# Kernel tuning notes

Hardware: AMD Instinct MI355X
Metric: run time of the kernel (lower is better)

## Reference

```python
import math
import jax, jax.numpy as jnp
import numpy as np

D_MODEL = 512
NHEAD = 8
D_HEAD = D_MODEL // NHEAD
ATTN_TEMP = 1.0
B, LQ, LK = 2, 2048, 4096


def _linear_params(key, d_in, d_out):
    kw, kb = jax.random.split(key)
    bound = 1.0 / math.sqrt(d_in)
    W = jax.random.uniform(kw, (d_out, d_in), jnp.float32, -bound, bound)
    b = jax.random.uniform(kb, (d_out,), jnp.float32, -bound, bound)
    return W, b


def setup_inputs() -> dict:
    key = jax.random.key(0)
    ks = jax.random.split(key, 8)
    q = jax.random.normal(ks[0], (B, LQ, D_MODEL), jnp.float32)
    kv = jax.random.normal(ks[1], (B, LK, D_MODEL), jnp.float32)
    key_gate = jax.random.uniform(ks[2], (B, LK), jnp.float32)
    key_mask = jax.random.randint(ks[3], (B, LK), 0, 2, jnp.int32)
    Wq, bq = _linear_params(ks[4], D_MODEL, D_MODEL)
    Wk, bk = _linear_params(ks[5], D_MODEL, D_MODEL)
    Wv, bv = _linear_params(ks[6], D_MODEL, D_MODEL)
    Wo, bo = _linear_params(ks[7], D_MODEL, D_MODEL)
    return {"q": q, "kv": kv, "key_gate": key_gate, "key_mask": key_mask,
            "Wq": Wq, "bq": bq, "Wk": Wk, "bk": bk,
            "Wv": Wv, "bv": bv, "Wo": Wo, "bo": bo}


def reference(q, kv, key_gate, key_mask, Wq, bq, Wk, bk, Wv, bv, Wo, bo):
    Bq, Lq, _ = q.shape
    _, Lk, _ = kv.shape
    # projections -> (B, H, L, Dh)
    qp = (q @ Wq.T + bq).reshape(Bq, Lq, NHEAD, D_HEAD).transpose(0, 2, 1, 3)
    kp = (kv @ Wk.T + bk).reshape(Bq, Lk, NHEAD, D_HEAD).transpose(0, 2, 1, 3)
    vp = (kv @ Wv.T + bv).reshape(Bq, Lk, NHEAD, D_HEAD).transpose(0, 2, 1, 3)
    # scores: (B, H, Lq, Lk)
    scores = jnp.einsum('bhqd,bhkd->bhqk', qp, kp) / (math.sqrt(D_HEAD) * ATTN_TEMP)
    log_gate = jnp.log(jnp.clip(key_gate, 1e-6, None))  # (B, Lk)
    scores = scores + log_gate[:, None, None, :]
    pad = (key_mask == 0)[:, None, None, :]
    scores = jnp.where(pad, -jnp.inf, scores)
    attn = jax.nn.softmax(scores, axis=-1)  # dropout is identity in eval
    out = jnp.einsum('bhqk,bhkd->bhqd', attn, vp)
    out = out.transpose(0, 2, 1, 3).reshape(Bq, Lq, D_MODEL)
    return out @ Wo.T + bo
```

## Files before the change

kernel.cpp:

```cpp
#include <hip/hip_runtime.h>
#include <hip/hip_bf16.h>


using bf16  = __hip_bfloat16;
using bf16x8 = __attribute__((ext_vector_type(8))) short;
using f32x4  = __attribute__((ext_vector_type(4))) float;

#define MFMA16(a, b, c) __builtin_amdgcn_mfma_f32_16x16x32_bf16((a), (b), (c), 0, 0, 0)

__device__ __forceinline__ bf16x8 load8(const bf16* p) {
    return *reinterpret_cast<const bf16x8*>(p);
}
__device__ __forceinline__ short f2bf(float x) {
    bf16 h = __float2bfloat16(x);
    return *reinterpret_cast<short*>(&h);
}

__global__ void cvt_x(const float* __restrict__ q, const float* __restrict__ kv,
                      bf16* __restrict__ qb, bf16* __restrict__ kvb) {
    int i = blockIdx.x * blockDim.x + threadIdx.x;
    const float* src; bf16* dst; int j;
    if (i < 524288) { src = q;  dst = qb;  j = i; }
    else            { src = kv; dst = kvb; j = i - 524288; }
    float4 v = reinterpret_cast<const float4*>(src)[j];
    ushort4 o;
    o.x = (unsigned short)f2bf(v.x);
    o.y = (unsigned short)f2bf(v.y);
    o.z = (unsigned short)f2bf(v.z);
    o.w = (unsigned short)f2bf(v.w);
    reinterpret_cast<ushort4*>(dst)[j] = o;
}

__global__ void cvt_w(const float* __restrict__ a, const float* __restrict__ b,
                      const float* __restrict__ c, const float* __restrict__ d,
                      bf16* __restrict__ oa, bf16* __restrict__ ob,
                      bf16* __restrict__ oc, bf16* __restrict__ od) {
    int i = blockIdx.x * blockDim.x + threadIdx.x;
    int t = i >> 16, j = i & 65535;
    const float* src = (t == 0) ? a : (t == 1) ? b : (t == 2) ? c : d;
    bf16*        dst = (t == 0) ? oa : (t == 1) ? ob : (t == 2) ? oc : od;
    float4 v = reinterpret_cast<const float4*>(src)[j];
    ushort4 o;
    o.x = (unsigned short)f2bf(v.x);
    o.y = (unsigned short)f2bf(v.y);
    o.z = (unsigned short)f2bf(v.z);
    o.w = (unsigned short)f2bf(v.w);
    reinterpret_cast<ushort4*>(dst)[j] = o;
}

__global__ void prep_gate_kernel(const float* __restrict__ gate,
                                 const int* __restrict__ mask,
                                 float* __restrict__ g, int n) {
    int i = blockIdx.x * blockDim.x + threadIdx.x;
    if (i < n) {
        float gv = fmaxf(gate[i], 1e-6f);
        g[i] = mask[i] ? logf(gv) : -1e30f;
    }
}

__device__ __forceinline__ void proj_body(const bf16* __restrict__ X,
                                          const bf16* __restrict__ W,
                                          const float* __restrict__ bias,
                                          void* __restrict__ Cout,
                                          int mode, int L, int mb, bf16* Ws) {
    const int tid  = threadIdx.x;
    const int wave = tid >> 6;
    const int lane = tid & 63;
    const int li   = lane & 15;
    const int quad = lane >> 4;
    const int n0   = blockIdx.x * 64;
    const int m0   = mb * 128 + wave * 32;

    f32x4 zero = {0.f, 0.f, 0.f, 0.f};
    f32x4 acc[2][4];
    for (int mt = 0; mt < 2; ++mt)
        for (int t = 0; t < 4; ++t) acc[mt][t] = zero;

    const bf16* x0 = X + (size_t)(m0 + li) * 512;
    const bf16* x1 = X + (size_t)(m0 + 16 + li) * 512;

    for (int p = 0; p < 2; ++p) {
        __syncthreads();
        for (int i = 0; i < 8; ++i) {
            const int c  = i * 256 + tid;
            const int cr = c >> 5;
            const int kc = (c & 31) * 8;
            *reinterpret_cast<bf16x8*>(&Ws[cr * 264 + kc]) =
                load8(W + (size_t)(n0 + cr) * 512 + p * 256 + kc);
        }
        __syncthreads();

        for (int k0 = 0; k0 < 256; k0 += 32) {
            bf16x8 a0 = load8(x0 + p * 256 + k0 + quad * 8);
            bf16x8 a1 = load8(x1 + p * 256 + k0 + quad * 8);
            for (int t = 0; t < 4; ++t) {
                bf16x8 w8 = load8(&Ws[(t * 16 + li) * 264 + k0 + quad * 8]);
                acc[0][t] = MFMA16(a0, w8, acc[0][t]);
                acc[1][t] = MFMA16(a1, w8, acc[1][t]);
            }
        }
    }

    for (int t = 0; t < 4; ++t) {
        const int col = n0 + t * 16 + li;
        const float bcol = bias[col];
        for (int mt = 0; mt < 2; ++mt) {
            for (int r = 0; r < 4; ++r) {
                const int row = m0 + mt * 16 + quad * 4 + r;
                const float v = acc[mt][t][r] + bcol;
                if (mode == 0) {
                    ((float*)Cout)[(size_t)row * 512 + col] = v;
                } else {
                    const int bb2 = row / L;
                    const int i   = row - bb2 * L;
                    const int hh  = col >> 6;
                    const int dh  = col & 63;
                    size_t idx;
                    if (mode == 1) idx = ((size_t)(bb2 * 8 + hh) * L + i) * 64 + dh;
                    else           idx = ((size_t)(bb2 * 8 + hh) * 64 + dh) * L + i;
                    ((bf16*)Cout)[idx] = __float2bfloat16(v);
                }
            }
        }
    }
}

__global__ void proj_qkv(const bf16* __restrict__ qb, const bf16* __restrict__ kvb,
                         const bf16* __restrict__ Wq, const float* __restrict__ bq,
                         const bf16* __restrict__ Wk, const float* __restrict__ bk,
                         const bf16* __restrict__ Wv, const float* __restrict__ bv,
                         bf16* __restrict__ qp, bf16* __restrict__ kp,
                         bf16* __restrict__ vpt) {
    __shared__ alignas(16) bf16 Ws[64 * 264];
    const int my = blockIdx.y;
    if (my < 32)      proj_body(qb,  Wq, bq, qp,  1, 2048, my,      Ws);
    else if (my < 96) proj_body(kvb, Wk, bk, kp,  1, 4096, my - 32, Ws);
    else              proj_body(kvb, Wv, bv, vpt, 2, 4096, my - 96, Ws);
}

__global__ void proj_o(const bf16* __restrict__ op, const bf16* __restrict__ Wo,
                       const float* __restrict__ bo, float* __restrict__ out) {
    __shared__ alignas(16) bf16 Ws[64 * 264];
    proj_body(op, Wo, bo, out, 0, 1, blockIdx.y, Ws);
}

#define PS 72
__global__ void attn_kernel(const bf16* __restrict__ qp, const bf16* __restrict__ kp,
                            const bf16* __restrict__ vpt, const float* __restrict__ g,
                            float* __restrict__ Opart, float* __restrict__ lpart) {
    __shared__ alignas(16) bf16 Kt[64 * PS];
    __shared__ alignas(16) bf16 Vt[64 * PS];
    __shared__ alignas(16) bf16 Pt[4 * 32 * PS];
    __shared__ float gs[64];

    const int tid  = threadIdx.x;
    const int wave = tid >> 6;
    const int lane = tid & 63;
    const int li   = lane & 15;
    const int quad = lane >> 4;

    const int bx = blockIdx.x;
    const int ks = bx & 3;
    const int qt = (bx >> 2) & 15;
    const int h  = (bx >> 6) & 7;
    const int b  = bx >> 9;
    const size_t bh = (size_t)(b * 8 + h);

    const bf16* qb0 = qp + (bh * 2048 + (size_t)qt * 128 + wave * 32 + li) * 64;
    bf16x8 aq[2][2];
    aq[0][0] = load8(qb0 + quad * 8);
    aq[0][1] = load8(qb0 + 32 + quad * 8);
    aq[1][0] = load8(qb0 + 16 * 64 + quad * 8);
    aq[1][1] = load8(qb0 + 16 * 64 + 32 + quad * 8);

    f32x4 zero = {0.f, 0.f, 0.f, 0.f};
    f32x4 o[2][4];
    for (int mt = 0; mt < 2; ++mt)
        for (int t = 0; t < 4; ++t) o[mt][t] = zero;
    float lsum[2][4] = {{0.f, 0.f, 0.f, 0.f}, {0.f, 0.f, 0.f, 0.f}};

    const bf16* ksrc  = kp  + bh * 4096 * 64;
    const bf16* vsrc  = vpt + bh * 64 * 4096;
    const float* gsrc = g + (size_t)b * 4096;

    bf16* PtW = &Pt[wave * 32 * PS];

    for (int kt = ks * 16; kt < ks * 16 + 16; ++kt) {
        {
            const int r0 = tid >> 3;
            const int cg = (tid & 7) * 8;
            const bf16* kst = ksrc + (size_t)kt * 64 * 64;
            *reinterpret_cast<bf16x8*>(&Kt[r0 * PS + cg])        = load8(kst + r0 * 64 + cg);
            *reinterpret_cast<bf16x8*>(&Kt[(r0 + 32) * PS + cg]) = load8(kst + (r0 + 32) * 64 + cg);
            const bf16* vs = vsrc + kt * 64;
            *reinterpret_cast<bf16x8*>(&Vt[r0 * PS + cg])        = load8(vs + (size_t)r0 * 4096 + cg);
            *reinterpret_cast<bf16x8*>(&Vt[(r0 + 32) * PS + cg]) = load8(vs + (size_t)(r0 + 32) * 4096 + cg);
            if (tid < 64) gs[tid] = gsrc[kt * 64 + tid];
        }
        __syncthreads();

        for (int t = 0; t < 4; ++t) {
            bf16x8 bk0 = load8(&Kt[(t * 16 + li) * PS + quad * 8]);
            bf16x8 bk1 = load8(&Kt[(t * 16 + li) * PS + 32 + quad * 8]);
            const float gv = gs[t * 16 + li];
            for (int mt = 0; mt < 2; ++mt) {
                f32x4 acc = zero;
                acc = MFMA16(aq[mt][0], bk0, acc);
                acc = MFMA16(aq[mt][1], bk1, acc);
                for (int r = 0; r < 4; ++r) {
                    const float p = __expf(acc[r] * 0.125f + gv);
                    lsum[mt][r] += p;
                    PtW[(mt * 16 + quad * 4 + r) * PS + t * 16 + li] = __float2bfloat16(p);
                }
            }
        }

        bf16x8 ap[2][2];
        ap[0][0] = load8(&PtW[li * PS + quad * 8]);
        ap[0][1] = load8(&PtW[li * PS + 32 + quad * 8]);
        ap[1][0] = load8(&PtW[(16 + li) * PS + quad * 8]);
        ap[1][1] = load8(&PtW[(16 + li) * PS + 32 + quad * 8]);
        for (int t = 0; t < 4; ++t) {
            bf16x8 bv0 = load8(&Vt[(t * 16 + li) * PS + quad * 8]);
            bf16x8 bv1 = load8(&Vt[(t * 16 + li) * PS + 32 + quad * 8]);
            for (int mt = 0; mt < 2; ++mt) {
                o[mt][t] = MFMA16(ap[mt][0], bv0, o[mt][t]);
                o[mt][t] = MFMA16(ap[mt][1], bv1, o[mt][t]);
            }
        }
        __syncthreads();
    }

    for (int off = 1; off < 16; off <<= 1)
        for (int mt = 0; mt < 2; ++mt)
            for (int r = 0; r < 4; ++r)
                lsum[mt][r] += __shfl_xor(lsum[mt][r], off);

    float* ob = Opart + ((size_t)bx * 128 + wave * 32) * 64;
    for (int mt = 0; mt < 2; ++mt)
        for (int t = 0; t < 4; ++t)
            for (int r = 0; r < 4; ++r)
                ob[(size_t)(mt * 16 + quad * 4 + r) * 64 + t * 16 + li] = o[mt][t][r];
    if (li == 0)
        for (int mt = 0; mt < 2; ++mt)
            for (int r = 0; r < 4; ++r)
                lpart[(size_t)bx * 128 + wave * 32 + mt * 16 + quad * 4 + r] = lsum[mt][r];
}

__global__ void attn_combine(const float* __restrict__ Opart,
                             const float* __restrict__ lpart,
                             bf16* __restrict__ op) {
    const int gidx = blockIdx.x * 256 + threadIdx.x;
    const int row  = gidx >> 2;
    const int c0   = (gidx & 3) * 16;
    const int b    = row >> 14;
    const int h    = (row >> 11) & 7;
    const int q    = row & 2047;
    const int qt   = q >> 7;
    const int r128 = q & 127;
    const int base = (((b * 8 + h) * 16) + qt) * 4;

    float acc[16];
    for (int j = 0; j < 16; ++j) acc[j] = 0.f;
    float L = 0.f;
    for (int s = 0; s < 4; ++s) {
        const float* src = Opart + ((size_t)(base + s) * 128 + r128) * 64 + c0;
        const float4 v0 = reinterpret_cast<const float4*>(src)[0];
        const float4 v1 = reinterpret_cast<const float4*>(src)[1];
        const float4 v2 = reinterpret_cast<const float4*>(src)[2];
        const float4 v3 = reinterpret_cast<const float4*>(src)[3];
        acc[0] += v0.x; acc[1] += v0.y; acc[2]  += v0.z; acc[3]  += v0.w;
        acc[4] += v1.x; acc[5] += v1.y; acc[6]  += v1.z; acc[7]  += v1.w;
        acc[8] += v2.x; acc[9] += v2.y; acc[10] += v2.z; acc[11] += v2.w;
        acc[12] += v3.x; acc[13] += v3.y; acc[14] += v3.z; acc[15] += v3.w;
        L += lpart[(size_t)(base + s) * 128 + r128];
    }
    const float invL = 1.0f / L;

    bf16* dst = op + ((size_t)b * 2048 + q) * 512 + h * 64 + c0;
    bf16x8 r0, r1;
    for (int j = 0; j < 8; ++j) {
        r0[j] = f2bf(acc[j] * invL);
        r1[j] = f2bf(acc[8 + j] * invL);
    }
    *reinterpret_cast<bf16x8*>(dst)     = r0;
    *reinterpret_cast<bf16x8*>(dst + 8) = r1;
}

extern "C" void kernel_launch(void* const* d_in, const int* in_sizes, int n_in,
                              void* d_out, int out_size, void* d_ws, size_t ws_size,
                              hipStream_t stream) {
    const float* q    = (const float*)d_in[0];
    const float* kv   = (const float*)d_in[1];
    const float* gate = (const float*)d_in[2];
    const int*   mask = (const int*)d_in[3];
    const float* Wq = (const float*)d_in[4];  const float* bq = (const float*)d_in[5];
    const float* Wk = (const float*)d_in[6];  const float* bk = (const float*)d_in[7];
    const float* Wv = (const float*)d_in[8];  const float* bv = (const float*)d_in[9];
    const float* Wo = (const float*)d_in[10]; const float* bo = (const float*)d_in[11];
    float* out = (float*)d_out;

    char* ws = (char*)d_ws;
    float* g   = (float*)ws;
    bf16* Wqb  = (bf16*)(ws + (1u  << 20));
    bf16* Wkb  = (bf16*)(ws + (1u  << 20) + (512u << 10));
    bf16* Wvb  = (bf16*)(ws + (2u  << 20));
    bf16* Wob  = (bf16*)(ws + (2u  << 20) + (512u << 10));
    bf16* qb   = (bf16*)(ws + (3u  << 20));
    bf16* kvb  = (bf16*)(ws + (7u  << 20));
    bf16* qp   = (bf16*)(ws + (15u << 20));
    bf16* kp   = (bf16*)(ws + (19u << 20));
    bf16* vpt  = (bf16*)(ws + (27u << 20));
    bf16* op   = (bf16*)(ws + (35u << 20));
    float* Opart = (float*)(ws + (39u << 20));
    float* lpart = (float*)(ws + (71u << 20));

    prep_gate_kernel<<<32, 256, 0, stream>>>(gate, mask, g, 2 * 4096);
    cvt_x<<<6144, 256, 0, stream>>>(q, kv, qb, kvb);
    cvt_w<<<1024, 256, 0, stream>>>(Wq, Wk, Wv, Wo, Wqb, Wkb, Wvb, Wob);

    proj_qkv<<<dim3(8, 160), 256, 0, stream>>>(qb, kvb, Wqb, bq, Wkb, bk,
                                               Wvb, bv, qp, kp, vpt);

    attn_kernel<<<1024, 256, 0, stream>>>(qp, kp, vpt, g, Opart, lpart);
    attn_combine<<<512, 256, 0, stream>>>(Opart, lpart, op);

    proj_o<<<dim3(8, 32), 256, 0, stream>>>(op, Wob, bo, out);
}
```

Before: 202.1 us.

## Rewrite attention with 32x32 MFMA, fragment-ordered K/V layouts and register-resident P

The projection kernel now writes K and V directly in MFMA fragment order, so the attention kernel loads operands straight from global memory into registers with no LDS staging and no block barriers. Attention switches to 32x32x16 MFMAs, computes S^T so P can be repacked in registers with cvt_pk_bf16 and permlane32_swap, and uses exp2 with a log2 gate. It prefetches the next K tile while running the PV MFMAs, and the partial-output layout changes so the combine kernel reads contiguous rows. The cost is higher register pressure, tied to launch_bounds of 2 blocks, and fewer blocks (512) each covering 256 queries.

```diff
diff --git a/kernel.cpp b/kernel.cpp
--- a/kernel.cpp
+++ b/kernel.cpp
@@ -2,11 +2,14 @@
 #include <hip/hip_bf16.h>
 
 
-using bf16  = __hip_bfloat16;
+using bf16   = __hip_bfloat16;
 using bf16x8 = __attribute__((ext_vector_type(8))) short;
 using f32x4  = __attribute__((ext_vector_type(4))) float;
+using f32x16 = __attribute__((ext_vector_type(16))) float;
+using uint4v = __attribute__((ext_vector_type(4))) unsigned int;
 
 #define MFMA16(a, b, c) __builtin_amdgcn_mfma_f32_16x16x32_bf16((a), (b), (c), 0, 0, 0)
+#define MFMA32(a, b, c) __builtin_amdgcn_mfma_f32_32x32x16_bf16((a), (b), (c), 0, 0, 0)
 
 __device__ __forceinline__ bf16x8 load8(const bf16* p) {
     return *reinterpret_cast<const bf16x8*>(p);
@@ -54,7 +57,7 @@
     int i = blockIdx.x * blockDim.x + threadIdx.x;
     if (i < n) {
         float gv = fmaxf(gate[i], 1e-6f);
-        g[i] = mask[i] ? logf(gv) : -1e30f;
+        g[i] = mask[i] ? log2f(gv) : -1e30f;
     }
 }
 
@@ -115,9 +118,18 @@
                     const int i   = row - bb2 * L;
                     const int hh  = col >> 6;
                     const int dh  = col & 63;
+                    const int bh  = bb2 * 8 + hh;
                     size_t idx;
-                    if (mode == 1) idx = ((size_t)(bb2 * 8 + hh) * L + i) * 64 + dh;
-                    else           idx = ((size_t)(bb2 * 8 + hh) * 64 + dh) * L + i;
+                    if (mode == 1) {
+                        idx = ((size_t)bh * L + i) * 64 + dh;
+                    } else if (mode == 3) {
+                        idx = ((((size_t)bh * 128 + (i >> 5)) * 4 + (dh >> 4)) * 64
+                               + ((dh >> 3) & 1) * 32 + (i & 31)) * 8 + (dh & 7);
+                    } else {
+                        idx = (((((size_t)bh * 128 + (i >> 5)) * 2 + (dh >> 5)) * 2
+                               + ((i >> 4) & 1)) * 64 + ((i >> 3) & 1) * 32 + (dh & 31)) * 8
+                              + (i & 7);
+                    }
                     ((bf16*)Cout)[idx] = __float2bfloat16(v);
                 }
             }
@@ -129,13 +141,13 @@
                          const bf16* __restrict__ Wq, const float* __restrict__ bq,
                          const bf16* __restrict__ Wk, const float* __restrict__ bk,
                          const bf16* __restrict__ Wv, const float* __restrict__ bv,
-                         bf16* __restrict__ qp, bf16* __restrict__ kp,
-                         bf16* __restrict__ vpt) {
+                         bf16* __restrict__ qp, bf16* __restrict__ kf,
+                         bf16* __restrict__ vf) {
     __shared__ alignas(16) bf16 Ws[64 * 264];
     const int my = blockIdx.y;
-    if (my < 32)      proj_body(qb,  Wq, bq, qp,  1, 2048, my,      Ws);
-    else if (my < 96) proj_body(kvb, Wk, bk, kp,  1, 4096, my - 32, Ws);
-    else              proj_body(kvb, Wv, bv, vpt, 2, 4096, my - 96, Ws);
+    if (my < 32)      proj_body(qb,  Wq, bq, qp, 1, 2048, my,      Ws);
+    else if (my < 96) proj_body(kvb, Wk, bk, kf, 3, 4096, my - 32, Ws);
+    else              proj_body(kvb, Wv, bv, vf, 4, 4096, my - 96, Ws);
 }
 
 __global__ void proj_o(const bf16* __restrict__ op, const bf16* __restrict__ Wo,
@@ -144,107 +156,143 @@
     proj_body(op, Wo, bo, out, 0, 1, blockIdx.y, Ws);
 }
 
-#define PS 72
-__global__ void attn_kernel(const bf16* __restrict__ qp, const bf16* __restrict__ kp,
-                            const bf16* __restrict__ vpt, const float* __restrict__ g,
-                            float* __restrict__ Opart, float* __restrict__ lpart) {
-    __shared__ alignas(16) bf16 Kt[64 * PS];
-    __shared__ alignas(16) bf16 Vt[64 * PS];
-    __shared__ alignas(16) bf16 Pt[4 * 32 * PS];
-    __shared__ float gs[64];
-
+__global__ __launch_bounds__(256, 2)
+void attn_kernel(const bf16* __restrict__ qp, const bf16* __restrict__ kf,
+                 const bf16* __restrict__ vf, const float* __restrict__ g2,
+                 float* __restrict__ Opart, float* __restrict__ lpart) {
     const int tid  = threadIdx.x;
     const int wave = tid >> 6;
     const int lane = tid & 63;
-    const int li   = lane & 15;
-    const int quad = lane >> 4;
+    const int ql   = lane & 31;
+    const int hi   = lane >> 5;
 
     const int bx = blockIdx.x;
-    const int ks = bx & 3;
-    const int qt = (bx >> 2) & 15;
-    const int h  = (bx >> 6) & 7;
-    const int b  = bx >> 9;
-    const size_t bh = (size_t)(b * 8 + h);
-
-    const bf16* qb0 = qp + (bh * 2048 + (size_t)qt * 128 + wave * 32 + li) * 64;
-    bf16x8 aq[2][2];
-    aq[0][0] = load8(qb0 + quad * 8);
-    aq[0][1] = load8(qb0 + 32 + quad * 8);
-    aq[1][0] = load8(qb0 + 16 * 64 + quad * 8);
-    aq[1][1] = load8(qb0 + 16 * 64 + 32 + quad * 8);
-
-    f32x4 zero = {0.f, 0.f, 0.f, 0.f};
-    f32x4 o[2][4];
-    for (int mt = 0; mt < 2; ++mt)
-        for (int t = 0; t < 4; ++t) o[mt][t] = zero;
-    float lsum[2][4] = {{0.f, 0.f, 0.f, 0.f}, {0.f, 0.f, 0.f, 0.f}};
-
-    const bf16* ksrc  = kp  + bh * 4096 * 64;
-    const bf16* vsrc  = vpt + bh * 64 * 4096;
-    const float* gsrc = g + (size_t)b * 4096;
-
-    bf16* PtW = &Pt[wave * 32 * PS];
-
-    for (int kt = ks * 16; kt < ks * 16 + 16; ++kt) {
-        {
-            const int r0 = tid >> 3;
-            const int cg = (tid & 7) * 8;
-            const bf16* kst = ksrc + (size_t)kt * 64 * 64;
-            *reinterpret_cast<bf16x8*>(&Kt[r0 * PS + cg])        = load8(kst + r0 * 64 + cg);
-            *reinterpret_cast<bf16x8*>(&Kt[(r0 + 32) * PS + cg]) = load8(kst + (r0 + 32) * 64 + cg);
-            const bf16* vs = vsrc + kt * 64;
-            *reinterpret_cast<bf16x8*>(&Vt[r0 * PS + cg])        = load8(vs + (size_t)r0 * 4096 + cg);
-            *reinterpret_cast<bf16x8*>(&Vt[(r0 + 32) * PS + cg]) = load8(vs + (size_t)(r0 + 32) * 4096 + cg);
-            if (tid < 64) gs[tid] = gsrc[kt * 64 + tid];
-        }
-        __syncthreads();
-
-        for (int t = 0; t < 4; ++t) {
-            bf16x8 bk0 = load8(&Kt[(t * 16 + li) * PS + quad * 8]);
-            bf16x8 bk1 = load8(&Kt[(t * 16 + li) * PS + 32 + quad * 8]);
-            const float gv = gs[t * 16 + li];
-            for (int mt = 0; mt < 2; ++mt) {
-                f32x4 acc = zero;
-                acc = MFMA16(aq[mt][0], bk0, acc);
-                acc = MFMA16(aq[mt][1], bk1, acc);
-                for (int r = 0; r < 4; ++r) {
-                    const float p = __expf(acc[r] * 0.125f + gv);
-                    lsum[mt][r] += p;
-                    PtW[(mt * 16 + quad * 4 + r) * PS + t * 16 + li] = __float2bfloat16(p);
-                }
+    const int sp = bx & 3;
+    const int qt = (bx >> 2) & 7;
+    const int h  = (bx >> 5) & 7;
+    const int b  = bx >> 8;
+    const int bh = b * 8 + h;
+    const int q0 = qt * 256 + wave * 64;
+
+    bf16x8 bq[2][4];
+    const bf16* qb = qp + ((size_t)bh * 2048 + q0 + ql) * 64 + hi * 8;
+    #pragma unroll
+    for (int sub = 0; sub < 2; ++sub)
+        #pragma unroll
+        for (int ds = 0; ds < 4; ++ds)
+            bq[sub][ds] = load8(qb + sub * 2048 + ds * 16);
+
+    f32x16 od[2][2];
+    #pragma unroll
+    for (int sub = 0; sub < 2; ++sub)
+        #pragma unroll
+        for (int t = 0; t < 2; ++t)
+            #pragma unroll
+            for (int r = 0; r < 16; ++r) od[sub][t][r] = 0.f;
+    float lsum[2] = {0.f, 0.f};
+
+    const bf16* kbase = kf + (size_t)bh * 262144 + (size_t)sp * 65536 + lane * 8;
+    const bf16* vbase = vf + (size_t)bh * 262144 + (size_t)sp * 65536 + lane * 8;
+    const float* gbase = g2 + (size_t)b * 4096 + sp * 1024 + hi * 4;
+
+    const float SC = 0.18033688011112042f;
+
+    bf16x8 ka0 = load8(kbase);
+    bf16x8 ka1 = load8(kbase + 512);
+    bf16x8 ka2 = load8(kbase + 1024);
+    bf16x8 ka3 = load8(kbase + 1536);
+
+    for (int kt = 0; kt < 32; ++kt) {
+        const bf16* vp = vbase + (size_t)kt * 2048;
+        bf16x8 bv00 = load8(vp);
+        bf16x8 bv01 = load8(vp + 512);
+        bf16x8 bv10 = load8(vp + 1024);
+        bf16x8 bv11 = load8(vp + 1536);
+        const float* gp = gbase + kt * 32;
+        f32x4 gv0 = *(const f32x4*)(gp);
+        f32x4 gv1 = *(const f32x4*)(gp + 8);
+        f32x4 gv2 = *(const f32x4*)(gp + 16);
+        f32x4 gv3 = *(const f32x4*)(gp + 24);
+        float gl[16];
+        #pragma unroll
+        for (int c = 0; c < 4; ++c) {
+            gl[c] = gv0[c]; gl[4 + c] = gv1[c]; gl[8 + c] = gv2[c]; gl[12 + c] = gv3[c];
+        }
+
+        bf16x8 pa[2][2];
+        #pragma unroll
+        for (int sub = 0; sub < 2; ++sub) {
+            f32x16 sacc;
+            #pragma unroll
+            for (int r = 0; r < 16; ++r) sacc[r] = 0.f;
+            sacc = MFMA32(ka0, bq[sub][0], sacc);
+            sacc = MFMA32(ka1, bq[sub][1], sacc);
+            sacc = MFMA32(ka2, bq[sub][2], sacc);
+            sacc = MFMA32(ka3, bq[sub][3], sacc);
+
+            float p[16];
+            #pragma unroll
+            for (int r = 0; r < 16; ++r)
+                p[r] = __builtin_amdgcn_exp2f(fmaf(sacc[r], SC, gl[r]));
+
+            unsigned w[8];
+            #pragma unroll
+            for (int i = 0; i < 8; ++i)
+                asm("v_cvt_pk_bf16_f32 %0, %1, %2"
+                    : "=v"(w[i]) : "v"(p[2 * i]), "v"(p[2 * i + 1]));
+
+            #pragma unroll
+            for (int st = 1; st < 16; st <<= 1)
+                #pragma unroll
+                for (int r = 0; r < 16; r += 2 * st) p[r] += p[r + st];
+            lsum[sub] += p[0];
+
+            asm("v_permlane32_swap_b32 %0, %1" : "+v"(w[0]), "+v"(w[2]));
+            asm("v_permlane32_swap_b32 %0, %1" : "+v"(w[1]), "+v"(w[3]));
+            asm("v_permlane32_swap_b32 %0, %1" : "+v"(w[4]), "+v"(w[6]));
+            asm("v_permlane32_swap_b32 %0, %1" : "+v"(w[5]), "+v"(w[7]));
+            uint4v u0 = {w[0], w[1], w[2], w[3]};
+            uint4v u1 = {w[4], w[5], w[6], w[7]};
+            pa[sub][0] = __builtin_bit_cast(bf16x8, u0);
+            pa[sub][1] = __builtin_bit_cast(bf16x8, u1);
+        }
+
+        const int ktn = kt < 31 ? kt + 1 : 31;
+        const bf16* kp_n = kbase + (size_t)ktn * 2048;
+        bf16x8 kn0 = load8(kp_n);
+        bf16x8 kn1 = load8(kp_n + 512);
+        bf16x8 kn2 = load8(kp_n + 1024);
+        bf16x8 kn3 = load8(kp_n + 1536);
+
+        od[0][0] = MFMA32(pa[0][0], bv00, od[0][0]);
+        od[0][0] = MFMA32(pa[0][1], bv01, od[0][0]);
+        od[0][1] = MFMA32(pa[0][0], bv10, od[0][1]);
+        od[0][1] = MFMA32(pa[0][1], bv11, od[0][1]);
+        od[1][0] = MFMA32(pa[1][0], bv00, od[1][0]);
+        od[1][0] = MFMA32(pa[1][1], bv01, od[1][0]);
+        od[1][1] = MFMA32(pa[1][0], bv10, od[1][1]);
+        od[1][1] = MFMA32(pa[1][1], bv11, od[1][1]);
+
+        ka0 = kn0; ka1 = kn1; ka2 = kn2; ka3 = kn3;
+    }
+
+    float l0 = lsum[0] + __shfl_xor(lsum[0], 32);
+    float l1 = lsum[1] + __shfl_xor(lsum[1], 32);
+
+    float* ob = Opart + ((size_t)(bh * 2048 + q0) * 4 + sp) * 64;
+    #pragma unroll
+    for (int sub = 0; sub < 2; ++sub)
+        #pragma unroll
+        for (int t = 0; t < 2; ++t)
+            #pragma unroll
+            for (int r = 0; r < 16; ++r) {
+                const int qq = sub * 32 + (r & 3) + 8 * (r >> 2) + hi * 4;
+                ob[(size_t)qq * 256 + t * 32 + ql] = od[sub][t][r];
             }
-        }
-
-        bf16x8 ap[2][2];
-        ap[0][0] = load8(&PtW[li * PS + quad * 8]);
-        ap[0][1] = load8(&PtW[li * PS + 32 + quad * 8]);
-        ap[1][0] = load8(&PtW[(16 + li) * PS + quad * 8]);
-        ap[1][1] = load8(&PtW[(16 + li) * PS + 32 + quad * 8]);
-        for (int t = 0; t < 4; ++t) {
-            bf16x8 bv0 = load8(&Vt[(t * 16 + li) * PS + quad * 8]);
-            bf16x8 bv1 = load8(&Vt[(t * 16 + li) * PS + 32 + quad * 8]);
-            for (int mt = 0; mt < 2; ++mt) {
-                o[mt][t] = MFMA16(ap[mt][0], bv0, o[mt][t]);
-                o[mt][t] = MFMA16(ap[mt][1], bv1, o[mt][t]);
-            }
-        }
-        __syncthreads();
-    }
-
-    for (int off = 1; off < 16; off <<= 1)
-        for (int mt = 0; mt < 2; ++mt)
-            for (int r = 0; r < 4; ++r)
-                lsum[mt][r] += __shfl_xor(lsum[mt][r], off);
-
-    float* ob = Opart + ((size_t)bx * 128 + wave * 32) * 64;
-    for (int mt = 0; mt < 2; ++mt)
-        for (int t = 0; t < 4; ++t)
-            for (int r = 0; r < 4; ++r)
-                ob[(size_t)(mt * 16 + quad * 4 + r) * 64 + t * 16 + li] = o[mt][t][r];
-    if (li == 0)
-        for (int mt = 0; mt < 2; ++mt)
-            for (int r = 0; r < 4; ++r)
-                lpart[(size_t)bx * 128 + wave * 32 + mt * 16 + quad * 4 + r] = lsum[mt][r];
+    if (lane < 32) {
+        lpart[((size_t)(bh * 2048 + q0 + lane)) * 4 + sp]      = l0;
+        lpart[((size_t)(bh * 2048 + q0 + 32 + lane)) * 4 + sp] = l1;
+    }
 }
 
 __global__ void attn_combine(const float* __restrict__ Opart,
@@ -253,18 +301,13 @@
     const int gidx = blockIdx.x * 256 + threadIdx.x;
     const int row  = gidx >> 2;
     const int c0   = (gidx & 3) * 16;
-    const int b    = row >> 14;
-    const int h    = (row >> 11) & 7;
-    const int q    = row & 2047;
-    const int qt   = q >> 7;
-    const int r128 = q & 127;
-    const int base = (((b * 8 + h) * 16) + qt) * 4;
 
     float acc[16];
+    #pragma unroll
     for (int j = 0; j < 16; ++j) acc[j] = 0.f;
     float L = 0.f;
     for (int s = 0; s < 4; ++s) {
-        const float* src = Opart + ((size_t)(base + s) * 128 + r128) * 64 + c0;
+        const float* src = Opart + ((size_t)row * 4 + s) * 64 + c0;
         const float4 v0 = reinterpret_cast<const float4*>(src)[0];
         const float4 v1 = reinterpret_cast<const float4*>(src)[1];
         const float4 v2 = reinterpret_cast<const float4*>(src)[2];
@@ -273,12 +316,17 @@
         acc[4] += v1.x; acc[5] += v1.y; acc[6]  += v1.z; acc[7]  += v1.w;
         acc[8] += v2.x; acc[9] += v2.y; acc[10] += v2.z; acc[11] += v2.w;
         acc[12] += v3.x; acc[13] += v3.y; acc[14] += v3.z; acc[15] += v3.w;
-        L += lpart[(size_t)(base + s) * 128 + r128];
+        L += lpart[(size_t)row * 4 + s];
     }
     const float invL = 1.0f / L;
 
-    bf16* dst = op + ((size_t)b * 2048 + q) * 512 + h * 64 + c0;
+    const int bh = row >> 11;
+    const int q  = row & 2047;
+    const int bb = bh >> 3;
+    const int hh = bh & 7;
+    bf16* dst = op + ((size_t)bb * 2048 + q) * 512 + hh * 64 + c0;
     bf16x8 r0, r1;
+    #pragma unroll
     for (int j = 0; j < 8; ++j) {
         r0[j] = f2bf(acc[j] * invL);
         r1[j] = f2bf(acc[8 + j] * invL);
@@ -301,7 +349,7 @@
     float* out = (float*)d_out;
 
     char* ws = (char*)d_ws;
-    float* g   = (float*)ws;
+    float* g2  = (float*)ws;
     bf16* Wqb  = (bf16*)(ws + (1u  << 20));
     bf16* Wkb  = (bf16*)(ws + (1u  << 20) + (512u << 10));
     bf16* Wvb  = (bf16*)(ws + (2u  << 20));
@@ -309,20 +357,20 @@
     bf16* qb   = (bf16*)(ws + (3u  << 20));
     bf16* kvb  = (bf16*)(ws + (7u  << 20));
     bf16* qp   = (bf16*)(ws + (15u << 20));
-    bf16* kp   = (bf16*)(ws + (19u << 20));
-    bf16* vpt  = (bf16*)(ws + (27u << 20));
+    bf16* kf   = (bf16*)(ws + (19u << 20));
+    bf16* vf   = (bf16*)(ws + (27u << 20));
     bf16* op   = (bf16*)(ws + (35u << 20));
     float* Opart = (float*)(ws + (39u << 20));
     float* lpart = (float*)(ws + (71u << 20));
 
-    prep_gate_kernel<<<32, 256, 0, stream>>>(gate, mask, g, 2 * 4096);
+    prep_gate_kernel<<<32, 256, 0, stream>>>(gate, mask, g2, 2 * 4096);
     cvt_x<<<6144, 256, 0, stream>>>(q, kv, qb, kvb);
     cvt_w<<<1024, 256, 0, stream>>>(Wq, Wk, Wv, Wo, Wqb, Wkb, Wvb, Wob);
 
     proj_qkv<<<dim3(8, 160), 256, 0, stream>>>(qb, kvb, Wqb, bq, Wkb, bk,
-                                               Wvb, bv, qp, kp, vpt);
-
-    attn_kernel<<<1024, 256, 0, stream>>>(qp, kp, vpt, g, Opart, lpart);
+                                               Wvb, bv, qp, kf, vf);
+
+    attn_kernel<<<512, 256, 0, stream>>>(qp, kf, vf, g2, Opart, lpart);
     attn_combine<<<512, 256, 0, stream>>>(Opart, lpart, op);
 
     proj_o<<<dim3(8, 32), 256, 0, stream>>>(op, Wob, bo, out);
```

Measured after the change: 189.7 us. 6.1% less time.
